# Optimization experiments

Hardware: AMD Instinct MI355X
Metric: run time of the kernel (lower is better)

## Reference

```python
import jax, jax.numpy as jnp
import numpy as np

N_WAY = 2
K_SHOT = 5
C = 320
NPTS = 2048
NQ = 2
K_PROTO = 100  # hardcoded k=100 in forward
N_CLS = N_WAY + 1
SIGMA = 1.0
NEG = -1e9


def _l2norm(x, eps=1e-8):
    return x / (jnp.linalg.norm(x, axis=-1, keepdims=True) + eps)


def _class_prototypes(feat, mask, k):
    """Multi-prototype masked pooling for one class.
    feat: [M, C] point features; mask: [M] float (1 = belongs to class).
    Picks k masked seed points, assigns every masked point to its
    nearest (cosine) seed, and returns the k masked cluster means.
    """
    M = feat.shape[0]
    # deterministic seeds: first k masked points (tie-break by index)
    score = mask - jnp.arange(M, dtype=feat.dtype) * 1e-9
    _, seed_idx = jax.lax.top_k(score, k)
    seeds = feat[seed_idx]                      # [k, C]
    sim = _l2norm(feat) @ _l2norm(seeds).T      # [M, k]
    assign = jnp.argmax(sim, axis=1)            # [M]
    onehot = jax.nn.one_hot(assign, k, dtype=feat.dtype) * mask[:, None]  # [M, k]
    num = onehot.T @ feat                       # [k, C]
    den = onehot.sum(axis=0)[:, None] + 1e-8
    return num / den


def _fg_prototypes(support_feat, fg_mask, k):
    # support_feat [n_way, k_shot, C, N] -> per-class point sets [n_way, k_shot*N, C]
    feat = support_feat.transpose(0, 1, 3, 2).reshape(N_WAY, -1, C)
    m = fg_mask.reshape(N_WAY, -1).astype(feat.dtype)
    protos = jax.vmap(lambda f, mm: _class_prototypes(f, mm, k))(feat, m)  # [n_way, k, C]
    labels = jnp.repeat(jnp.arange(1, N_WAY + 1), k)                        # classes 1..n_way
    return protos.reshape(-1, C), jax.nn.one_hot(labels, N_CLS, dtype=feat.dtype)


def _bg_prototypes(support_feat, bg_mask, k):
    feat = support_feat.transpose(0, 1, 3, 2).reshape(-1, C)   # all shots pooled
    m = bg_mask.reshape(-1).astype(feat.dtype)
    protos = _class_prototypes(feat, m, k)                      # [k, C]
    labels = jnp.zeros((k,), dtype=jnp.int32)                   # class 0 = background
    return protos, jax.nn.one_hot(labels, N_CLS, dtype=feat.dtype)


def _predict(prototypes, proto_onehot, qfeat, qlabels):
    # cosine similarity [M, P], per-class max over that class's prototypes
    sim = (_l2norm(qfeat) @ _l2norm(prototypes).T) / SIGMA        # [M, P]
    cls_mask = proto_onehot.T[None] > 0                            # [1, ncls, P]
    pred = jnp.max(jnp.where(cls_mask, sim[:, None, :], NEG), axis=-1)  # [M, ncls]
    logp = jax.nn.log_softmax(pred, axis=-1)
    loss = -jnp.mean(jnp.take_along_axis(logp, qlabels.reshape(-1, 1), axis=1))
    query_pred = pred.reshape(NQ, NPTS, N_CLS).transpose(0, 2, 1)  # [NQ, ncls, NPTS]
    return loss, query_pred


def reference(support_feat, query_feat, support_y, query_y):
    fg_mask = support_y
    bg_mask = 1 - support_y
    fg_protos, fg_labels = _fg_prototypes(support_feat, fg_mask, K_PROTO)
    bg_protos, bg_labels = _bg_prototypes(support_feat, bg_mask, K_PROTO)
    prototypes = jnp.concatenate([bg_protos, fg_protos], axis=0)           # [P, C]
    proto_labels = jnp.concatenate([bg_labels, fg_labels], axis=0)         # [P, ncls]

    qfeat = query_feat.transpose(0, 2, 1).reshape(-1, C)                   # [NQ*NPTS, C]
    loss, query_pred = _predict(prototypes, proto_labels, qfeat, query_y)
    # the forward adds computeCrossEntropyLoss(query_pred, query_y): same CE again
    loss = loss * 2.0

    # post-hoc per-point confidence thresholding (vectorized Python loop)
    qp = jnp.concatenate([query_pred[0], query_pred[1]], axis=-1)          # [ncls, NQ*NPTS]
    predictions = jnp.argmax(qp, axis=0)
    confidences = jnp.max(qp, axis=0)
    final = jnp.where(confidences > jnp.mean(confidences), predictions, -1)
    final_labels = jnp.stack([final[:NPTS], final[NPTS:]], axis=0)         # [2, NPTS]
    return loss, query_pred, final_labels


def setup_inputs() -> dict:
    key = jax.random.key(0)
    k1, k2, k3, k4 = jax.random.split(key, 4)
    return {
        "support_feat": jax.random.normal(k1, (N_WAY, K_SHOT, C, NPTS), dtype=jnp.float32),
        "query_feat": jax.random.normal(k2, (NQ, C, NPTS), dtype=jnp.float32),
        "support_y": jax.random.randint(k3, (N_WAY, K_SHOT, NPTS), 0, 2, dtype=jnp.int32),
        "query_y": jax.random.randint(k4, (NQ, NPTS), 0, 3, dtype=jnp.int32),
    }
```

## Files before the change

### kernel.cpp

```cpp
#include <hip/hip_runtime.h>
#include <math.h>

#define C 320
#define NPTS 2048
#define SUPPTS 20480
#define QPTS 4096
#define KP 100
#define NCLS 3
#define PSTRIDE 300

__global__ __launch_bounds__(64) void k_protoseed(const float* __restrict__ sup,
                                                  const int* __restrict__ sy,
                                                  float* __restrict__ pbufT) {
    int p    = blockIdx.x;
    int lane = threadIdx.x;
    int prob = (p < 100) ? 2 : ((p < 200) ? 0 : 1);
    int rank = (p < 100) ? p : ((p < 200) ? p - 100 : p - 200);
    int M    = (prob == 2) ? SUPPTS : 10240;
    int base = (prob == 1) ? 10240 : 0;
    int found = 0, sp = 0;
    for (int chunk = 0; chunk < M; chunk += 64) {
        int yy = sy[base + chunk + lane];
        int m  = (prob == 2) ? (1 - yy) : yy;
        unsigned long long bal = __ballot(m != 0);
        int cnt = __popcll(bal);
        if (found + cnt > rank) {
            int need = rank - found;
            int prefix = __popcll(bal & ((1ull << lane) - 1ull));
            unsigned long long match = __ballot(m && (prefix == need));
            int pos = __ffsll((unsigned long long)match) - 1;
            sp = base + chunk + pos;
            break;
        }
        found += cnt;
    }
    const float* fb = sup + ((size_t)(sp >> 11) * C) * NPTS + (sp & 2047);
    float v[5]; float s = 0.f;
    #pragma unroll
    for (int i = 0; i < 5; i++) {
        v[i] = fb[(size_t)(lane + i * 64) * NPTS];
        s += v[i] * v[i];
    }
    #pragma unroll
    for (int off = 32; off > 0; off >>= 1) s += __shfl_down(s, off);
    s = __shfl(s, 0);
    float r = 1.0f / (sqrtf(s) + 1e-8f);
    #pragma unroll
    for (int i = 0; i < 5; i++)
        pbufT[(size_t)(lane + i * 64) * PSTRIDE + p] = v[i] * r;
}

__global__ __launch_bounds__(128) void k_assign(const float* __restrict__ sup,
                                                const float* __restrict__ pbT,
                                                float* __restrict__ pmaxv,
                                                int* __restrict__ pmaxj) {
    __shared__ float shp[C * 20];
    int b = blockIdx.x, jt = blockIdx.y, tid = threadIdx.x;
    int prob, pt, gbase, aoff;
    if (b < 40)       { prob = 0; pt = b * 256;         gbase = 0;     aoff = 0; }
    else if (b < 80)  { prob = 1; pt = (b - 40) * 256;  gbase = 10240; aoff = 10240; }
    else              { prob = 2; pt = (b - 80) * 256;  gbase = 0;     aoff = 20480; }
    int j0 = jt * 20;
    int col0 = (prob == 2) ? 0 : (100 + prob * 100);
    for (int i = tid; i < C * 20; i += 128) {
        int j = i % 20, c = i / 20;
        shp[i] = pbT[(size_t)c * PSTRIDE + col0 + j0 + j];
    }
    __syncthreads();
    int g = gbase + pt + tid * 2;
    const float* fb = sup + ((size_t)(g >> 11) * C) * NPTS + (g & 2047);
    float acc0[20], acc1[20];
    #pragma unroll
    for (int j = 0; j < 20; j++) { acc0[j] = 0.f; acc1[j] = 0.f; }
    float2 pf[8];
    #pragma unroll
    for (int k = 0; k < 8; k++) pf[k] = *(const float2*)(fb + (size_t)k * NPTS);
    for (int cc = 0; cc < C; cc += 8) {
        float2 cur[8];
        #pragma unroll
        for (int k = 0; k < 8; k++) cur[k] = pf[k];
        if (cc + 8 < C) {
            #pragma unroll
            for (int k = 0; k < 8; k++) pf[k] = *(const float2*)(fb + (size_t)(cc + 8 + k) * NPTS);
        }
        #pragma unroll
        for (int k = 0; k < 8; k++) {
            const float4* r = (const float4*)&shp[(cc + k) * 20];
            float4 a = r[0], d1 = r[1], d2 = r[2], d3 = r[3], d4 = r[4];
            float px = cur[k].x, py = cur[k].y;
            acc0[0]+=px*a.x;  acc1[0]+=py*a.x;  acc0[1]+=px*a.y;  acc1[1]+=py*a.y;
            acc0[2]+=px*a.z;  acc1[2]+=py*a.z;  acc0[3]+=px*a.w;  acc1[3]+=py*a.w;
            acc0[4]+=px*d1.x; acc1[4]+=py*d1.x; acc0[5]+=px*d1.y; acc1[5]+=py*d1.y;
            acc0[6]+=px*d1.z; acc1[6]+=py*d1.z; acc0[7]+=px*d1.w; acc1[7]+=py*d1.w;
            acc0[8]+=px*d2.x; acc1[8]+=py*d2.x; acc0[9]+=px*d2.y; acc1[9]+=py*d2.y;
            acc0[10]+=px*d2.z;acc1[10]+=py*d2.z;acc0[11]+=px*d2.w;acc1[11]+=py*d2.w;
            acc0[12]+=px*d3.x;acc1[12]+=py*d3.x;acc0[13]+=px*d3.y;acc1[13]+=py*d3.y;
            acc0[14]+=px*d3.z;acc1[14]+=py*d3.z;acc0[15]+=px*d3.w;acc1[15]+=py*d3.w;
            acc0[16]+=px*d4.x;acc1[16]+=py*d4.x;acc0[17]+=px*d4.y;acc1[17]+=py*d4.y;
            acc0[18]+=px*d4.z;acc1[18]+=py*d4.z;acc0[19]+=px*d4.w;acc1[19]+=py*d4.w;
        }
    }
    float bv0 = acc0[0]; int bj0 = 0;
    float bv1 = acc1[0]; int bj1 = 0;
    #pragma unroll
    for (int j = 1; j < 20; j++) {
        if (acc0[j] > bv0) { bv0 = acc0[j]; bj0 = j; }
        if (acc1[j] > bv1) { bv1 = acc1[j]; bj1 = j; }
    }
    size_t a0 = (size_t)(aoff + pt + tid * 2) * 5 + jt;
    pmaxv[a0]     = bv0; pmaxj[a0]     = j0 + bj0;
    pmaxv[a0 + 5] = bv1; pmaxj[a0 + 5] = j0 + bj1;
}

__global__ __launch_bounds__(256) void k_combine_dst(const float* __restrict__ pmaxv,
                                                     const int* __restrict__ pmaxj,
                                                     const int* __restrict__ sy,
                                                     int* __restrict__ dst,
                                                     float* __restrict__ loss) {
    int g = blockIdx.x * 256 + threadIdx.x;
    if (g == 0) loss[0] = 0.f;
    float bvf = pmaxv[(size_t)g * 5]; int bjf = pmaxj[(size_t)g * 5];
    #pragma unroll
    for (int t = 1; t < 5; t++) {
        float v = pmaxv[(size_t)g * 5 + t];
        if (v > bvf) { bvf = v; bjf = pmaxj[(size_t)g * 5 + t]; }
    }
    size_t gb = (size_t)(SUPPTS + g) * 5;
    float bvb = pmaxv[gb]; int bjb = pmaxj[gb];
    #pragma unroll
    for (int t = 1; t < 5; t++) {
        float v = pmaxv[gb + t];
        if (v > bvb) { bvb = v; bjb = pmaxj[gb + t]; }
    }
    int way = (g >= 10240) ? 1 : 0;
    dst[g] = sy[g] ? (100 + way * 100 + bjf) : bjb;
}

__global__ __launch_bounds__(256) void k_accum_lds(const float* __restrict__ sup,
                                                   const int* __restrict__ dst,
                                                   float* __restrict__ part,
                                                   float* __restrict__ cnt) {
    __shared__ float bins[8 * 200];
    __shared__ float scnt[200];
    int bx = blockIdx.x;
    int ct = blockIdx.y;
    int tid = threadIdx.x;
    int ws = bx >> 1, half = bx & 1;
    int w = (ws >= 5) ? 1 : 0;
    int nbase = half * 1024;
    for (int i = tid; i < 8 * 200; i += 256) bins[i] = 0.f;
    if (ct == 0 && tid < 200) scnt[tid] = 0.f;
    int dreg[4];
    #pragma unroll
    for (int sub = 0; sub < 4; sub++) {
        int d = dst[ws * 2048 + nbase + sub * 256 + tid];
        dreg[sub] = (d < 100) ? d : (d - w * 100);
    }
    __syncthreads();
    if (ct == 0) {
        #pragma unroll
        for (int sub = 0; sub < 4; sub++) atomicAdd(&scnt[dreg[sub]], 1.0f);
    }
    const float* base = sup + ((size_t)ws * C + ct * 8) * NPTS + nbase;
    for (int cl = 0; cl < 8; cl++) {
        const float* row = base + (size_t)cl * NPTS;
        #pragma unroll
        for (int sub = 0; sub < 4; sub++)
            atomicAdd(&bins[cl * 200 + dreg[sub]], row[sub * 256 + tid]);
    }
    __syncthreads();
    float* pout = part + (size_t)(bx * 40 + ct) * 1600;
    for (int i = tid; i < 8 * 200; i += 256) {
        int bin = i >> 3, cl = i & 7;
        pout[i] = bins[cl * 200 + bin];
    }
    if (ct == 0 && tid < 200) cnt[bx * 200 + tid] = scnt[tid];
}

__global__ __launch_bounds__(64) void k_reduce_proto(const float* __restrict__ part,
                                                     const float* __restrict__ cnt,
                                                     float* __restrict__ phatT) {
    int d   = blockIdx.x;
    int tid = threadIdx.x;
    int local, s0, ns;
    if (d < 100)      { local = d;       s0 = 0;  ns = 20; }
    else if (d < 200) { local = d;       s0 = 0;  ns = 10; }
    else              { local = d - 100; s0 = 10; ns = 10; }
    float dn = 0.f;
    for (int k = 0; k < ns; k++) dn += cnt[(s0 + k) * 200 + local];
    float inv = 1.0f / (dn + 1e-8f);
    float vals[5]; float sq = 0.f;
    #pragma unroll
    for (int i = 0; i < 5; i++) {
        int c = tid + i * 64;
        int ct = c >> 3, cl = c & 7;
        float s = 0.f;
        for (int k = 0; k < ns; k++)
            s += part[(size_t)((s0 + k) * 40 + ct) * 1600 + local * 8 + cl];
        float v = s * inv;
        vals[i] = v; sq += v * v;
    }
    #pragma unroll
    for (int off = 32; off > 0; off >>= 1) sq += __shfl_down(sq, off);
    sq = __shfl(sq, 0);
    float rn = 1.0f / (sqrtf(sq) + 1e-8f);
    #pragma unroll
    for (int i = 0; i < 5; i++)
        phatT[(size_t)(tid + i * 64) * PSTRIDE + d] = vals[i] * rn;
}

__global__ __launch_bounds__(256) void k_qpartial(const float* __restrict__ qry,
                                                  const float* __restrict__ phT,
                                                  float* __restrict__ qmaxv,
                                                  float* __restrict__ qrn) {
    __shared__ float shp[C * 16];
    __shared__ float red[3 * 64 * 45];
    int pb = blockIdx.x, jt = blockIdx.y, tid = threadIdx.x;
    int wave = tid >> 6, lane = tid & 63;
    int j0 = jt * 10;
    for (int i = tid; i < C * 10; i += 256) {
        int j = i % 10, c = i / 10;
        shp[c * 16 + j] = phT[(size_t)c * PSTRIDE + j0 + j];
    }
    __syncthreads();
    int m = pb * 256 + lane * 4;
    int c0 = wave * 80;
    const float* fb = qry + ((size_t)(m >> 11) * C + c0) * NPTS + (m & 2047);
    float acc[4][10];
    #pragma unroll
    for (int p = 0; p < 4; p++)
        #pragma unroll
        for (int j = 0; j < 10; j++) acc[p][j] = 0.f;
    float qn[4] = {0.f, 0.f, 0.f, 0.f};
    float4 pf[8];
    #pragma unroll
    for (int k = 0; k < 8; k++) pf[k] = *(const float4*)(fb + (size_t)k * NPTS);
    for (int cc = 0; cc < 80; cc += 8) {
        float4 cur[8];
        #pragma unroll
        for (int k = 0; k < 8; k++) cur[k] = pf[k];
        if (cc + 8 < 80) {
            #pragma unroll
            for (int k = 0; k < 8; k++) pf[k] = *(const float4*)(fb + (size_t)(cc + 8 + k) * NPTS);
        }
        #pragma unroll
        for (int k = 0; k < 8; k++) {
            const float* row = &shp[(c0 + cc + k) * 16];
            float4 p0 = ((const float4*)row)[0];
            float4 p1 = ((const float4*)row)[1];
            float2 p2 = ((const float2*)row)[4];
            float pr[10] = {p0.x,p0.y,p0.z,p0.w,p1.x,p1.y,p1.z,p1.w,p2.x,p2.y};
            float4 cv = cur[k];
            if (jt == 0) {
                qn[0] += cv.x*cv.x; qn[1] += cv.y*cv.y; qn[2] += cv.z*cv.z; qn[3] += cv.w*cv.w;
            }
            #pragma unroll
            for (int j = 0; j < 10; j++) {
                acc[0][j] += cv.x * pr[j];
                acc[1][j] += cv.y * pr[j];
                acc[2][j] += cv.z * pr[j];
                acc[3][j] += cv.w * pr[j];
            }
        }
    }
    if (wave > 0) {
        float* my = red + ((wave - 1) * 64 + lane) * 45;
        #pragma unroll
        for (int p = 0; p < 4; p++)
            #pragma unroll
            for (int j = 0; j < 10; j++) my[p * 10 + j] = acc[p][j];
        #pragma unroll
        for (int p = 0; p < 4; p++) my[40 + p] = qn[p];
    }
    __syncthreads();
    if (wave == 0) {
        #pragma unroll
        for (int w = 0; w < 3; w++) {
            const float* my = red + (w * 64 + lane) * 45;
            #pragma unroll
            for (int p = 0; p < 4; p++)
                #pragma unroll
                for (int j = 0; j < 10; j++) acc[p][j] += my[p * 10 + j];
            #pragma unroll
            for (int p = 0; p < 4; p++) qn[p] += my[40 + p];
        }
        #pragma unroll
        for (int p = 0; p < 4; p++) {
            float bv = acc[p][0];
            #pragma unroll
            for (int j = 1; j < 10; j++) bv = fmaxf(bv, acc[p][j]);
            qmaxv[(size_t)(m + p) * 30 + jt] = bv;
        }
        if (jt == 0) {
            #pragma unroll
            for (int p = 0; p < 4; p++) qrn[m + p] = 1.0f / (sqrtf(qn[p]) + 1e-8f);
        }
    }
}

__global__ __launch_bounds__(256) void k_pred(const float* __restrict__ qmaxv,
                                              const float* __restrict__ qrn,
                                              const int* __restrict__ qy,
                                              float* __restrict__ out,
                                              float* __restrict__ lossacc) {
    int m = blockIdx.x * 256 + threadIdx.x;
    float rn = qrn[m];
    float pred[NCLS];
    #pragma unroll
    for (int cls = 0; cls < NCLS; cls++) {
        float g = qmaxv[(size_t)m * 30 + cls * 10];
        #pragma unroll
        for (int t = 1; t < 10; t++) g = fmaxf(g, qmaxv[(size_t)m * 30 + cls * 10 + t]);
        pred[cls] = rn * g;
    }
    int q = m >> 11, n = m & 2047;
    #pragma unroll
    for (int cls = 0; cls < NCLS; cls++)
        out[1 + ((size_t)(q * NCLS + cls)) * NPTS + n] = pred[cls];
    float mx = fmaxf(pred[0], fmaxf(pred[1], pred[2]));
    float lse = mx + logf(expf(pred[0] - mx) + expf(pred[1] - mx) + expf(pred[2] - mx));
    int lab = qy[m];
    atomicAdd(lossacc, lse - pred[lab]);
}

__global__ __launch_bounds__(1024) void k_final(float* __restrict__ out,
                                                const float* __restrict__ lossacc) {
    __shared__ float red[1024];
    const float* pr = out + 1;
    int tid = threadIdx.x;
    float conf[4]; int lab[4];
    float s = 0.f;
    #pragma unroll
    for (int i = 0; i < 4; i++) {
        int m = tid + i * 1024;
        int q = m >> 11, n = m & 2047;
        float p0 = pr[((size_t)(q * NCLS + 0)) * NPTS + n];
        float p1 = pr[((size_t)(q * NCLS + 1)) * NPTS + n];
        float p2 = pr[((size_t)(q * NCLS + 2)) * NPTS + n];
        int l = 0; float c = p0;
        if (p1 > c) { c = p1; l = 1; }
        if (p2 > c) { c = p2; l = 2; }
        conf[i] = c; lab[i] = l; s += c;
    }
    red[tid] = s; __syncthreads();
    for (int off = 512; off > 0; off >>= 1) {
        if (tid < off) red[tid] += red[tid + off];
        __syncthreads();
    }
    float mean = red[0] / (float)QPTS;
    #pragma unroll
    for (int i = 0; i < 4; i++) {
        int m = tid + i * 1024;
        out[1 + 2 * NCLS * NPTS + m] = (conf[i] > mean) ? (float)lab[i] : -1.0f;
    }
    if (tid == 0) out[0] = 2.0f * lossacc[0] / (float)QPTS;
}

extern "C" void kernel_launch(void* const* d_in, const int* in_sizes, int n_in,
                              void* d_out, int out_size, void* d_ws, size_t ws_size,
                              hipStream_t stream) {
    const float* sup = (const float*)d_in[0];
    const float* qry = (const float*)d_in[1];
    const int*   sy  = (const int*)d_in[2];
    const int*   qy  = (const int*)d_in[3];
    float* out = (float*)d_out;

    float* f      = (float*)d_ws;
    float* qrn    = f;
    float* cnt    = qrn + QPTS;
    float* pbufT  = cnt + 4000;
    float* phatT  = pbufT + 96000;
    float* loss   = phatT + 96000;
    int*   dstb   = (int*)(loss + 4);
    float* trans  = (float*)(dstb + SUPPTS);
    float* pmaxv  = trans;
    int*   pmaxj  = (int*)(pmaxv + 204800);
    float* part   = trans;
    float* qmaxv  = trans;

    k_protoseed<<<300, 64, 0, stream>>>(sup, sy, pbufT);
    {
        dim3 grid(160, 5);
        k_assign<<<grid, 128, 0, stream>>>(sup, pbufT, pmaxv, pmaxj);
    }
    k_combine_dst<<<80, 256, 0, stream>>>(pmaxv, pmaxj, sy, dstb, loss);
    {
        dim3 grid(20, 40);
        k_accum_lds<<<grid, 256, 0, stream>>>(sup, dstb, part, cnt);
    }
    k_reduce_proto<<<300, 64, 0, stream>>>(part, cnt, phatT);
    {
        dim3 grid(16, 30);
        k_qpartial<<<grid, 256, 0, stream>>>(qry, phatT, qmaxv, qrn);
    }
    k_pred<<<16, 256, 0, stream>>>(qmaxv, qrn, qy, out, loss);
    k_final<<<1, 1024, 0, stream>>>(out, loss);
}
```

Before: 237.5 us.

## Transpose partial-max layout, replicate LDS bins, and reduce loss per block

The partial argmax buffer is switched from point-major with stride 5 to tile-major, so reads in the combine kernel and writes in the assign kernel become contiguous. The LDS histogram in the accumulate kernel is replicated four ways by thread index, which spreads shared-memory atomic contention across copies, at the cost of more LDS and an extra summation pass. The prediction kernel now reduces loss and confidence sums within each block, issuing one atomic per block instead of one per thread. Confidence and label are written to scratch so the final thresholding can run across 16 blocks instead of a single block.

```diff
diff --git a/kernel.cpp b/kernel.cpp
--- a/kernel.cpp
+++ b/kernel.cpp
@@ -107,9 +107,9 @@
         if (acc0[j] > bv0) { bv0 = acc0[j]; bj0 = j; }
         if (acc1[j] > bv1) { bv1 = acc1[j]; bj1 = j; }
     }
-    size_t a0 = (size_t)(aoff + pt + tid * 2) * 5 + jt;
+    size_t a0 = (size_t)jt * 40960 + (aoff + pt + tid * 2);
     pmaxv[a0]     = bv0; pmaxj[a0]     = j0 + bj0;
-    pmaxv[a0 + 5] = bv1; pmaxj[a0 + 5] = j0 + bj1;
+    pmaxv[a0 + 1] = bv1; pmaxj[a0 + 1] = j0 + bj1;
 }
 
 __global__ __launch_bounds__(256) void k_combine_dst(const float* __restrict__ pmaxv,
@@ -119,18 +119,18 @@
                                                      float* __restrict__ loss) {
     int g = blockIdx.x * 256 + threadIdx.x;
     if (g == 0) loss[0] = 0.f;
-    float bvf = pmaxv[(size_t)g * 5]; int bjf = pmaxj[(size_t)g * 5];
+    if (g == 1) loss[1] = 0.f;
+    float bvf = pmaxv[g]; int bjf = pmaxj[g];
     #pragma unroll
     for (int t = 1; t < 5; t++) {
-        float v = pmaxv[(size_t)g * 5 + t];
-        if (v > bvf) { bvf = v; bjf = pmaxj[(size_t)g * 5 + t]; }
-    }
-    size_t gb = (size_t)(SUPPTS + g) * 5;
-    float bvb = pmaxv[gb]; int bjb = pmaxj[gb];
+        float v = pmaxv[(size_t)t * 40960 + g];
+        if (v > bvf) { bvf = v; bjf = pmaxj[(size_t)t * 40960 + g]; }
+    }
+    float bvb = pmaxv[SUPPTS + g]; int bjb = pmaxj[SUPPTS + g];
     #pragma unroll
     for (int t = 1; t < 5; t++) {
-        float v = pmaxv[gb + t];
-        if (v > bvb) { bvb = v; bjb = pmaxj[gb + t]; }
+        float v = pmaxv[(size_t)t * 40960 + SUPPTS + g];
+        if (v > bvb) { bvb = v; bjb = pmaxj[(size_t)t * 40960 + SUPPTS + g]; }
     }
     int way = (g >= 10240) ? 1 : 0;
     dst[g] = sy[g] ? (100 + way * 100 + bjf) : bjb;
@@ -140,16 +140,17 @@
                                                    const int* __restrict__ dst,
                                                    float* __restrict__ part,
                                                    float* __restrict__ cnt) {
-    __shared__ float bins[8 * 200];
-    __shared__ float scnt[200];
+    __shared__ float bins[8 * 800];
+    __shared__ float scnt[800];
     int bx = blockIdx.x;
     int ct = blockIdx.y;
     int tid = threadIdx.x;
+    int copy = tid & 3;
     int ws = bx >> 1, half = bx & 1;
     int w = (ws >= 5) ? 1 : 0;
     int nbase = half * 1024;
-    for (int i = tid; i < 8 * 200; i += 256) bins[i] = 0.f;
-    if (ct == 0 && tid < 200) scnt[tid] = 0.f;
+    for (int i = tid; i < 8 * 800; i += 256) bins[i] = 0.f;
+    if (ct == 0) { for (int i = tid; i < 800; i += 256) scnt[i] = 0.f; }
     int dreg[4];
     #pragma unroll
     for (int sub = 0; sub < 4; sub++) {
@@ -159,22 +160,25 @@
     __syncthreads();
     if (ct == 0) {
         #pragma unroll
-        for (int sub = 0; sub < 4; sub++) atomicAdd(&scnt[dreg[sub]], 1.0f);
+        for (int sub = 0; sub < 4; sub++) atomicAdd(&scnt[copy * 200 + dreg[sub]], 1.0f);
     }
     const float* base = sup + ((size_t)ws * C + ct * 8) * NPTS + nbase;
     for (int cl = 0; cl < 8; cl++) {
         const float* row = base + (size_t)cl * NPTS;
         #pragma unroll
         for (int sub = 0; sub < 4; sub++)
-            atomicAdd(&bins[cl * 200 + dreg[sub]], row[sub * 256 + tid]);
+            atomicAdd(&bins[cl * 800 + copy * 200 + dreg[sub]], row[sub * 256 + tid]);
     }
     __syncthreads();
     float* pout = part + (size_t)(bx * 40 + ct) * 1600;
     for (int i = tid; i < 8 * 200; i += 256) {
         int bin = i >> 3, cl = i & 7;
-        pout[i] = bins[cl * 200 + bin];
-    }
-    if (ct == 0 && tid < 200) cnt[bx * 200 + tid] = scnt[tid];
+        float s = bins[cl * 800 + bin] + bins[cl * 800 + 200 + bin]
+                + bins[cl * 800 + 400 + bin] + bins[cl * 800 + 600 + bin];
+        pout[i] = s;
+    }
+    if (ct == 0 && tid < 200)
+        cnt[bx * 200 + tid] = scnt[tid] + scnt[200 + tid] + scnt[400 + tid] + scnt[600 + tid];
 }
 
 __global__ __launch_bounds__(64) void k_reduce_proto(const float* __restrict__ part,
@@ -302,8 +306,13 @@
                                               const float* __restrict__ qrn,
                                               const int* __restrict__ qy,
                                               float* __restrict__ out,
-                                              float* __restrict__ lossacc) {
-    int m = blockIdx.x * 256 + threadIdx.x;
+                                              float* __restrict__ lossacc,
+                                              float* __restrict__ cbuf,
+                                              int* __restrict__ lbuf) {
+    __shared__ float redL[256];
+    __shared__ float redC[256];
+    int tid = threadIdx.x;
+    int m = blockIdx.x * 256 + tid;
     float rn = qrn[m];
     float pred[NCLS];
     #pragma unroll
@@ -319,41 +328,32 @@
         out[1 + ((size_t)(q * NCLS + cls)) * NPTS + n] = pred[cls];
     float mx = fmaxf(pred[0], fmaxf(pred[1], pred[2]));
     float lse = mx + logf(expf(pred[0] - mx) + expf(pred[1] - mx) + expf(pred[2] - mx));
-    int lab = qy[m];
-    atomicAdd(lossacc, lse - pred[lab]);
-}
-
-__global__ __launch_bounds__(1024) void k_final(float* __restrict__ out,
-                                                const float* __restrict__ lossacc) {
-    __shared__ float red[1024];
-    const float* pr = out + 1;
-    int tid = threadIdx.x;
-    float conf[4]; int lab[4];
-    float s = 0.f;
-    #pragma unroll
-    for (int i = 0; i < 4; i++) {
-        int m = tid + i * 1024;
-        int q = m >> 11, n = m & 2047;
-        float p0 = pr[((size_t)(q * NCLS + 0)) * NPTS + n];
-        float p1 = pr[((size_t)(q * NCLS + 1)) * NPTS + n];
-        float p2 = pr[((size_t)(q * NCLS + 2)) * NPTS + n];
-        int l = 0; float c = p0;
-        if (p1 > c) { c = p1; l = 1; }
-        if (p2 > c) { c = p2; l = 2; }
-        conf[i] = c; lab[i] = l; s += c;
-    }
-    red[tid] = s; __syncthreads();
-    for (int off = 512; off > 0; off >>= 1) {
-        if (tid < off) red[tid] += red[tid + off];
+    int lab = 0; float cf = pred[0];
+    if (pred[1] > cf) { cf = pred[1]; lab = 1; }
+    if (pred[2] > cf) { cf = pred[2]; lab = 2; }
+    cbuf[m] = cf; lbuf[m] = lab;
+    redL[tid] = lse - pred[qy[m]];
+    redC[tid] = cf;
+    __syncthreads();
+    for (int off = 128; off > 0; off >>= 1) {
+        if (tid < off) { redL[tid] += redL[tid + off]; redC[tid] += redC[tid + off]; }
         __syncthreads();
     }
-    float mean = red[0] / (float)QPTS;
-    #pragma unroll
-    for (int i = 0; i < 4; i++) {
-        int m = tid + i * 1024;
-        out[1 + 2 * NCLS * NPTS + m] = (conf[i] > mean) ? (float)lab[i] : -1.0f;
-    }
-    if (tid == 0) out[0] = 2.0f * lossacc[0] / (float)QPTS;
+    if (tid == 0) {
+        atomicAdd(&lossacc[0], redL[0]);
+        atomicAdd(&lossacc[1], redC[0]);
+    }
+}
+
+__global__ __launch_bounds__(256) void k_final(const float* __restrict__ cbuf,
+                                               const int* __restrict__ lbuf,
+                                               const float* __restrict__ lossacc,
+                                               float* __restrict__ out) {
+    int m = blockIdx.x * 256 + threadIdx.x;
+    float mean = lossacc[1] / (float)QPTS;
+    float cf = cbuf[m];
+    out[1 + 2 * NCLS * NPTS + m] = (cf > mean) ? (float)lbuf[m] : -1.0f;
+    if (m == 0) out[0] = 2.0f * lossacc[0] / (float)QPTS;
 }
 
 extern "C" void kernel_launch(void* const* d_in, const int* in_sizes, int n_in,
@@ -377,6 +377,8 @@
     int*   pmaxj  = (int*)(pmaxv + 204800);
     float* part   = trans;
     float* qmaxv  = trans;
+    float* cbuf   = qmaxv + 122880;
+    int*   lbuf   = (int*)(cbuf + QPTS);
 
     k_protoseed<<<300, 64, 0, stream>>>(sup, sy, pbufT);
     {
@@ -393,6 +395,6 @@
         dim3 grid(16, 30);
         k_qpartial<<<grid, 256, 0, stream>>>(qry, phatT, qmaxv, qrn);
     }
-    k_pred<<<16, 256, 0, stream>>>(qmaxv, qrn, qy, out, loss);
-    k_final<<<1, 1024, 0, stream>>>(out, loss);
-}
+    k_pred<<<16, 256, 0, stream>>>(qmaxv, qrn, qy, out, loss, cbuf, lbuf);
+    k_final<<<16, 256, 0, stream>>>(cbuf, lbuf, loss, out);
+}
```

New measurement: 237.0 us. No clear change (-0.2%).
